# Kernel tuning notes

Measured on AMD Instinct MI355X. Metric: run time of the kernel, lower is better.

Reference implementation:

```python
import jax, jax.numpy as jnp
import numpy as np

EMB = 512
H = 8
D = EMB // H
N_TOK = 2048
IN_EMB = 1024
SCALE = EMB ** 0.5  # note: original divides AFTER softmax
EPS = 1e-5


def _layer_norm(x, g, b):
    m = x.mean(-1, keepdims=True)
    v = ((x - m) ** 2).mean(-1, keepdims=True)
    return (x - m) / jnp.sqrt(v + EPS) * g + b


def _mhla(x, idx, Wq, bq, Wk, bk, Wv, bv):
    # x: [b, n, EMB]; idx: [n, k] int neighbor indices into token axis
    b, n, _ = x.shape
    def heads(y):
        return y.reshape(b, n, H, D).transpose(0, 2, 1, 3)  # b h n d
    q = heads(x @ Wq + bq)
    k = heads(x @ Wk + bk)
    v = heads(x @ Wv + bv)
    Kl = k[:, :, idx, :]  # b h n k d  (gather of local keys)
    Vl = v[:, :, idx, :]  # b h n k d
    energy = jnp.einsum('bhnd,bhnkd->bhnk', q, Kl)
    att = jax.nn.softmax(energy, axis=-1) / SCALE  # faithful: scale after softmax
    patch_att = att.sum(axis=(1, 3)).T  # [n, b] (sum over heads, neighbors; stacked over n)
    out = jnp.einsum('bhnk,bhnkd->bhnd', att, Vl)
    out = out.transpose(0, 2, 1, 3).reshape(b, n, EMB)
    return out, patch_att


def setup_inputs() -> dict:
    key = jax.random.key(0)
    ks = jax.random.split(key, 16)
    def p(k, shape, s=0.02):
        return jax.random.normal(k, shape, dtype=jnp.float32) * s
    inp = {
        'x': jax.random.normal(ks[0], (1, N_TOK, IN_EMB), dtype=jnp.float32),
        'A': jax.random.randint(ks[1], (1, N_TOK, 64), 0, N_TOK),
        'W_fc': p(ks[2], (IN_EMB, EMB)), 'b_fc': jnp.zeros((EMB,), jnp.float32),
        'Wq1': p(ks[3], (EMB, EMB)), 'bq1': jnp.zeros((EMB,), jnp.float32),
        'Wk1': p(ks[4], (EMB, EMB)), 'bk1': jnp.zeros((EMB,), jnp.float32),
        'Wv1': p(ks[5], (EMB, EMB)), 'bv1': jnp.zeros((EMB,), jnp.float32),
        'g1': jnp.ones((EMB,), jnp.float32), 'be1': jnp.zeros((EMB,), jnp.float32),
        'Wq2': p(ks[6], (EMB, EMB)), 'bq2': jnp.zeros((EMB,), jnp.float32),
        'Wk2': p(ks[7], (EMB, EMB)), 'bk2': jnp.zeros((EMB,), jnp.float32),
        'Wv2': p(ks[8], (EMB, EMB)), 'bv2': jnp.zeros((EMB,), jnp.float32),
        'g2': jnp.ones((EMB,), jnp.float32), 'be2': jnp.zeros((EMB,), jnp.float32),
    }
    return inp


def reference(x, A, W_fc, b_fc, Wq1, bq1, Wk1, bk1, Wv1, bv1, g1, be1,
              Wq2, bq2, Wk2, bk2, Wv2, bv2, g2, be2):
    embs = jax.nn.relu(x @ W_fc + b_fc)  # FeedForwardBlock (dropout p=0)
    idx = A[0]  # batch==1 as required by torch.squeeze semantics in original
    b1, _ = _mhla(embs, idx[:, :16], Wq1, bq1, Wk1, bk1, Wv1, bv1)
    b1 = _layer_norm(b1 + embs, g1, be1)
    b2, Att2 = _mhla(b1, idx[:, :64], Wq2, bq2, Wk2, bk2, Wv2, bv2)
    b2 = _layer_norm(b2 + b1, g2, be2)
    return b2, Att2
```

## Files before the change

kernel.cpp:

```cpp
#include <hip/hip_runtime.h>

#define SCALE 22.627416997969522f
#define LNEPS 1e-5f
#define NTOK 2048

using short8 = __attribute__((ext_vector_type(8))) short;
using f32x4  = __attribute__((ext_vector_type(4))) float;
typedef unsigned short u16;
using u16x4 = __attribute__((ext_vector_type(4))) u16;

static __device__ __forceinline__ u16 f2bf(float f){
  unsigned u = __builtin_bit_cast(unsigned, f);
  u += 0x7FFFu + ((u >> 16) & 1u);
  return (u16)(u >> 16);
}
static __device__ __forceinline__ float bf2f(u16 u){
  unsigned v = ((unsigned)u) << 16;
  return __builtin_bit_cast(float, v);
}

__global__ __launch_bounds__(256) void cvt_k(const float* __restrict__ src,
                                             u16* __restrict__ dst, int n)
{
  int i = (blockIdx.x * 256 + threadIdx.x) * 4;
  if (i >= n) return;
  float4 v = *(const float4*)(src + i);
  u16x4 o;
  o[0] = f2bf(v.x); o[1] = f2bf(v.y); o[2] = f2bf(v.z); o[3] = f2bf(v.w);
  *(u16x4*)(dst + i) = o;
}

__global__ __launch_bounds__(256) void tr_k(
    const float* __restrict__ Wfc,
    const float* __restrict__ W1, const float* __restrict__ W2,
    const float* __restrict__ W3, const float* __restrict__ W4,
    const float* __restrict__ W5, const float* __restrict__ W6,
    u16* __restrict__ Tfc,
    u16* __restrict__ T1, u16* __restrict__ T2, u16* __restrict__ T3,
    u16* __restrict__ T4, u16* __restrict__ T5, u16* __restrict__ T6)
{
  int z = blockIdx.z;
  const float* W; u16* T; int K, N;
  if (z == 0) { W = Wfc; T = Tfc; K = 1024; N = 512; }
  else {
    K = 512; N = 512;
    switch (z) {
      case 1: W = W1; T = T1; break;
      case 2: W = W2; T = T2; break;
      case 3: W = W3; T = T3; break;
      case 4: W = W4; T = T4; break;
      case 5: W = W5; T = T5; break;
      default: W = W6; T = T6; break;
    }
    if ((int)blockIdx.y >= 16) return;
  }
  __shared__ float tile[32][33];
  int n0 = blockIdx.x * 32, k0 = blockIdx.y * 32;
  int tx = threadIdx.x & 31, ty = threadIdx.x >> 5;
#pragma unroll
  for (int i = 0; i < 32; i += 8)
    tile[ty + i][tx] = W[(size_t)(k0 + ty + i) * N + n0 + tx];
  __syncthreads();
#pragma unroll
  for (int i = 0; i < 32; i += 8)
    T[(size_t)(n0 + ty + i) * K + k0 + tx] = f2bf(tile[tx][ty + i]);
}

template<bool RELU, bool SPLIT3>
__global__ __launch_bounds__(256) void gemm_k(
    const u16* __restrict__ A, int K,
    const u16* __restrict__ T0, const u16* __restrict__ T1, const u16* __restrict__ T2,
    const float* __restrict__ B0, const float* __restrict__ B1, const float* __restrict__ B2,
    float* __restrict__ C0f, u16* __restrict__ C0b,
    u16* __restrict__ C1, u16* __restrict__ C2)
{
  __shared__ u16 As[64*64];
  __shared__ u16 Bs[64*64];

  int bm = blockIdx.x;
  int nglob = blockIdx.y * 64;
  int sel  = SPLIT3 ? (nglob >> 9) : 0;
  int ncol = nglob & 511;
  const u16*   T  = (sel==0) ? T0 : (sel==1) ? T1 : T2;
  const float* Bv = (sel==0) ? B0 : (sel==1) ? B1 : B2;

  int t = threadIdx.x;
  int wave = t >> 6, lane = t & 63;
  int wm = (wave >> 1) * 32, wn = (wave & 1) * 32;
  int lr = lane & 15, kg = lane >> 4;

  int o0 = t*16, o1 = 4096 + t*16;
  int r0 = o0 >> 7, cb0 = o0 & 127;
  int r1 = o1 >> 7, cb1 = o1 & 127;
  const char* Ag0 = (const char*)(A + (size_t)(bm*64 + r0) * K) + cb0;
  const char* Ag1 = (const char*)(A + (size_t)(bm*64 + r1) * K) + cb1;
  const char* Bg0 = (const char*)(T + (size_t)(ncol  + r0) * K) + cb0;
  const char* Bg1 = (const char*)(T + (size_t)(ncol  + r1) * K) + cb1;
  char* Ad0 = (char*)As + r0*128 + (cb0 ^ ((r0 & 7) << 4));
  char* Ad1 = (char*)As + r1*128 + (cb1 ^ ((r1 & 7) << 4));
  char* Bd0 = (char*)Bs + r0*128 + (cb0 ^ ((r0 & 7) << 4));
  char* Bd1 = (char*)Bs + r1*128 + (cb1 ^ ((r1 & 7) << 4));

  int sw = (lr & 7) << 4;
  const char* Afr0 = (const char*)As + (wm + lr) * 128;
  const char* Afr1 = (const char*)As + (wm + 16 + lr) * 128;
  const char* Bfr0 = (const char*)Bs + (wn + lr) * 128;
  const char* Bfr1 = (const char*)Bs + (wn + 16 + lr) * 128;

  f32x4 acc[2][2] = {};

  short8 pa0 = *(const short8*)Ag0;
  short8 pa1 = *(const short8*)Ag1;
  short8 pb0 = *(const short8*)Bg0;
  short8 pb1 = *(const short8*)Bg1;

  for (int k0 = 0; k0 < K; k0 += 64) {
    __syncthreads();
    *(short8*)Ad0 = pa0;  *(short8*)Ad1 = pa1;
    *(short8*)Bd0 = pb0;  *(short8*)Bd1 = pb1;
    __syncthreads();
    int kn = k0 + 64;
    if (kn < K) {
      pa0 = *(const short8*)(Ag0 + kn*2);
      pa1 = *(const short8*)(Ag1 + kn*2);
      pb0 = *(const short8*)(Bg0 + kn*2);
      pb1 = *(const short8*)(Bg1 + kn*2);
    }
#pragma unroll
    for (int ks = 0; ks < 2; ++ks) {
      int cb = (ks*64 + kg*16) ^ sw;
      short8 af0 = *(const short8*)(Afr0 + cb);
      short8 af1 = *(const short8*)(Afr1 + cb);
      short8 bf0 = *(const short8*)(Bfr0 + cb);
      short8 bf1 = *(const short8*)(Bfr1 + cb);
      acc[0][0] = __builtin_amdgcn_mfma_f32_16x16x32_bf16(af0, bf0, acc[0][0], 0, 0, 0);
      acc[0][1] = __builtin_amdgcn_mfma_f32_16x16x32_bf16(af0, bf1, acc[0][1], 0, 0, 0);
      acc[1][0] = __builtin_amdgcn_mfma_f32_16x16x32_bf16(af1, bf0, acc[1][0], 0, 0, 0);
      acc[1][1] = __builtin_amdgcn_mfma_f32_16x16x32_bf16(af1, bf1, acc[1][1], 0, 0, 0);
    }
  }

#pragma unroll
  for (int mi = 0; mi < 2; ++mi)
#pragma unroll
    for (int ni = 0; ni < 2; ++ni) {
      int col = ncol + wn + ni*16 + lr;
      float bia = Bv[col];
#pragma unroll
      for (int r = 0; r < 4; ++r) {
        int row = bm*64 + wm + mi*16 + kg*4 + r;
        float vv = acc[mi][ni][r] + bia;
        if (RELU) vv = fmaxf(vv, 0.f);
        if (SPLIT3) {
          if (sel == 0) {
            C0b[(size_t)row*512 + col] = f2bf(vv);
          } else {
            u16* C = (sel == 1) ? C1 : C2;
            C[((size_t)(col >> 6) * NTOK + row) * 64 + (col & 63)] = f2bf(vv);
          }
        } else {
          C0f[(size_t)row*512 + col] = vv;
          C0b[(size_t)row*512 + col] = f2bf(vv);
        }
      }
    }
}

template<int KLOC>
__global__ __launch_bounds__(512, 4) void attn_k(
    const u16* __restrict__ Qb, const u16* __restrict__ Kh, const u16* __restrict__ Vh,
    const int* __restrict__ Aidx,
    const float* __restrict__ resid,
    const float* __restrict__ gma, const float* __restrict__ bta,
    float* __restrict__ outp, u16* __restrict__ outb, float* __restrict__ attOut)
{
  constexpr int NP = KLOC / 16;
  constexpr int NV = KLOC / 8;

  __shared__ float o_s[512];
  __shared__ int   idx_s[KLOC];
  __shared__ float red_s[16];

  int n = blockIdx.x;
  int t = threadIdx.x;
  int w = t >> 6;
  int lane = t & 63;

  if (t < KLOC) idx_s[t] = Aidx[(size_t)n*64 + t];
  __syncthreads();

  const u16* Kbase = Kh + (size_t)w * NTOK * 64;
  const u16* Vbase = Vh + (size_t)w * NTOK * 64;
  int jj = lane & 15, dq = lane >> 4;
  int jg = lane >> 3, dc = lane & 7;

  short8 vpre[NV];
#pragma unroll
  for (int p = 0; p < NV; ++p)
    vpre[p] = *(const short8*)(Vbase + (size_t)idx_s[p*8 + jg] * 64 + dc*8);

  float qreg[16];
  {
    const u16* qp = Qb + (size_t)n*512 + w*64 + dq*16;
    short8 qa = *(const short8*)qp;
    short8 qb2 = *(const short8*)(qp + 8);
#pragma unroll
    for (int i = 0; i < 8; ++i) {
      qreg[i]     = bf2f((u16)qa[i]);
      qreg[8 + i] = bf2f((u16)qb2[i]);
    }
  }

  float att[NP];
#pragma unroll
  for (int p = 0; p < NP; ++p) {
    const u16* kp = Kbase + (size_t)idx_s[p*16 + jj] * 64 + dq*16;
    short8 k0 = *(const short8*)kp;
    short8 k1 = *(const short8*)(kp + 8);
    float e = 0.f;
#pragma unroll
    for (int i = 0; i < 8; ++i) {
      e = fmaf(qreg[i],     bf2f((u16)k0[i]), e);
      e = fmaf(qreg[8 + i], bf2f((u16)k1[i]), e);
    }
    e += __shfl_xor(e, 16);
    e += __shfl_xor(e, 32);
    att[p] = e;
  }

  float mx = att[0];
#pragma unroll
  for (int p = 1; p < NP; ++p) mx = fmaxf(mx, att[p]);
  mx = fmaxf(mx, __shfl_xor(mx, 1)); mx = fmaxf(mx, __shfl_xor(mx, 2));
  mx = fmaxf(mx, __shfl_xor(mx, 4)); mx = fmaxf(mx, __shfl_xor(mx, 8));
  float s = 0.f;
#pragma unroll
  for (int p = 0; p < NP; ++p) { att[p] = __expf(att[p] - mx); s += att[p]; }
  s += __shfl_xor(s, 1); s += __shfl_xor(s, 2);
  s += __shfl_xor(s, 4); s += __shfl_xor(s, 8);
  float inv = 1.f / (s * SCALE);
#pragma unroll
  for (int p = 0; p < NP; ++p) att[p] *= inv;

  float vacc[8] = {0.f,0.f,0.f,0.f,0.f,0.f,0.f,0.f};
#pragma unroll
  for (int p = 0; p < NV; ++p) {
    float a = __shfl(att[p >> 1], (p & 1) * 8 + jg);
#pragma unroll
    for (int i = 0; i < 8; ++i)
      vacc[i] = fmaf(a, bf2f((u16)vpre[p][i]), vacc[i]);
  }
#pragma unroll
  for (int i = 0; i < 8; ++i) {
    vacc[i] += __shfl_xor(vacc[i], 8);
    vacc[i] += __shfl_xor(vacc[i], 16);
    vacc[i] += __shfl_xor(vacc[i], 32);
  }
  if (jg == 0) {
#pragma unroll
    for (int i = 0; i < 8; ++i)
      o_s[w*64 + dc*8 + i] = vacc[i];
  }
  __syncthreads();

  float x = o_s[t] + __builtin_nontemporal_load(resid + (size_t)n*512 + t);
  float su = x, sq = x * x;
  su += __shfl_xor(su, 1);  sq += __shfl_xor(sq, 1);
  su += __shfl_xor(su, 2);  sq += __shfl_xor(sq, 2);
  su += __shfl_xor(su, 4);  sq += __shfl_xor(sq, 4);
  su += __shfl_xor(su, 8);  sq += __shfl_xor(sq, 8);
  su += __shfl_xor(su, 16); sq += __shfl_xor(sq, 16);
  su += __shfl_xor(su, 32); sq += __shfl_xor(sq, 32);
  if (lane == 0) { red_s[w] = su; red_s[8 + w] = sq; }
  __syncthreads();
  float tot = 0.f, tots = 0.f;
#pragma unroll
  for (int i = 0; i < 8; ++i) { tot += red_s[i]; tots += red_s[8 + i]; }
  float mean = tot  * (1.0f/512.0f);
  float var  = tots * (1.0f/512.0f) - mean*mean;
  float rstd = rsqrtf(var + LNEPS);
  float y = (x - mean) * rstd * gma[t] + bta[t];
  __builtin_nontemporal_store(y, outp + (size_t)n*512 + t);
  if (outb != nullptr) outb[(size_t)n*512 + t] = f2bf(y);
  if (attOut != nullptr && t == 0) attOut[n] = 8.0f / SCALE;
}

extern "C" void kernel_launch(void* const* d_in, const int* in_sizes, int n_in,
                              void* d_out, int out_size, void* d_ws, size_t ws_size,
                              hipStream_t stream)
{
  const float* x   = (const float*)d_in[0];
  const int*   A   = (const int*)  d_in[1];
  const float* Wfc = (const float*)d_in[2];
  const float* bfc = (const float*)d_in[3];
  const float* Wq1 = (const float*)d_in[4];
  const float* bq1 = (const float*)d_in[5];
  const float* Wk1 = (const float*)d_in[6];
  const float* bk1 = (const float*)d_in[7];
  const float* Wv1 = (const float*)d_in[8];
  const float* bv1 = (const float*)d_in[9];
  const float* g1  = (const float*)d_in[10];
  const float* be1 = (const float*)d_in[11];
  const float* Wq2 = (const float*)d_in[12];
  const float* bq2 = (const float*)d_in[13];
  const float* Wk2 = (const float*)d_in[14];
  const float* bk2 = (const float*)d_in[15];
  const float* Wv2 = (const float*)d_in[16];
  const float* bv2 = (const float*)d_in[17];
  const float* g2  = (const float*)d_in[18];
  const float* be2 = (const float*)d_in[19];

  char* ws = (char*)d_ws;
  const size_t SZ = (size_t)NTOK*512;
  float* embs = (float*)ws;                    ws += SZ*4;
  float* b1   = (float*)ws;                    ws += SZ*4;
  u16* embs_b = (u16*)ws;                      ws += SZ*2;
  u16* b1_b   = (u16*)ws;                      ws += SZ*2;
  u16* qb     = (u16*)ws;                      ws += SZ*2;
  u16* kb     = (u16*)ws;                      ws += SZ*2;
  u16* vb     = (u16*)ws;                      ws += SZ*2;
  u16* xb     = (u16*)ws;                      ws += (size_t)NTOK*1024*2;
  u16* t_fc   = (u16*)ws;                      ws += (size_t)512*1024*2;
  u16* t_q1   = (u16*)ws;                      ws += (size_t)512*512*2;
  u16* t_k1   = (u16*)ws;                      ws += (size_t)512*512*2;
  u16* t_v1   = (u16*)ws;                      ws += (size_t)512*512*2;
  u16* t_q2   = (u16*)ws;                      ws += (size_t)512*512*2;
  u16* t_k2   = (u16*)ws;                      ws += (size_t)512*512*2;
  u16* t_v2   = (u16*)ws;                      ws += (size_t)512*512*2;

  float* out  = (float*)d_out;
  float* att2 = out + SZ;

  dim3 blk(256);
  cvt_k<<<dim3(2048), blk, 0, stream>>>(x, xb, NTOK*1024);
  tr_k<<<dim3(16, 32, 7), blk, 0, stream>>>(Wfc, Wq1, Wk1, Wv1, Wq2, Wk2, Wv2,
      t_fc, t_q1, t_k1, t_v1, t_q2, t_k2, t_v2);

  gemm_k<true,false><<<dim3(32, 8), blk, 0, stream>>>(xb, 1024,
      t_fc, nullptr, nullptr, bfc, nullptr, nullptr, embs, embs_b, nullptr, nullptr);
  gemm_k<false,true><<<dim3(32, 24), blk, 0, stream>>>(embs_b, 512,
      t_q1, t_k1, t_v1, bq1, bk1, bv1, nullptr, qb, kb, vb);
  attn_k<16><<<dim3(2048), dim3(512), 0, stream>>>(qb, kb, vb, A, embs, g1, be1, b1, b1_b, nullptr);
  gemm_k<false,true><<<dim3(32, 24), blk, 0, stream>>>(b1_b, 512,
      t_q2, t_k2, t_v2, bq2, bk2, bv2, nullptr, qb, kb, vb);
  attn_k<64><<<dim3(2048), dim3(512), 0, stream>>>(qb, kb, vb, A, b1, g2, be2, out, nullptr, att2);
}
```

Baseline: 172.2 us.

## Fuse all stages into one persistent megakernel with software grid barriers

Replaces the seven separate kernel launches (convert, transpose, three GEMMs, two attention passes) with a single persistent kernel of 256 blocks that runs each stage in turn, separated by atomic-counter grid barriers. Each 512-thread block runs two independent 256-thread GEMM engines, and each block handles 8 tokens per attention stage. Separate q/k/v buffers are added for the second layer. The aim is to remove launch gaps and tail effects between the small stages. In exchange it adds spin-barrier overhead, a memset launch, and lower parallelism in the attention stages (256 blocks instead of 2048, with occupancy hint 2 instead of 4). It also relies on all 256 blocks being co-resident.

```diff
diff --git a/kernel.cpp b/kernel.cpp
--- a/kernel.cpp
+++ b/kernel.cpp
@@ -3,6 +3,7 @@
 #define SCALE 22.627416997969522f
 #define LNEPS 1e-5f
 #define NTOK 2048
+#define NBLK 256
 
 using short8 = __attribute__((ext_vector_type(8))) short;
 using f32x4  = __attribute__((ext_vector_type(4))) float;
@@ -19,77 +20,46 @@
   return __builtin_bit_cast(float, v);
 }
 
-__global__ __launch_bounds__(256) void cvt_k(const float* __restrict__ src,
-                                             u16* __restrict__ dst, int n)
+struct MegaArgs {
+  const float* x; const int* A;
+  const float* Wfc; const float* bfc;
+  const float* Wq1; const float* bq1; const float* Wk1; const float* bk1;
+  const float* Wv1; const float* bv1; const float* g1;  const float* be1;
+  const float* Wq2; const float* bq2; const float* Wk2; const float* bk2;
+  const float* Wv2; const float* bv2; const float* g2;  const float* be2;
+  unsigned* ctr;
+  float* embs; u16* embs_b; float* b1; u16* b1_b;
+  u16* xb;
+  u16* qb; u16* kb; u16* vb;
+  u16* qb2; u16* kb2; u16* vb2;
+  u16* t_fc; u16* t_q1; u16* t_k1; u16* t_v1; u16* t_q2; u16* t_k2; u16* t_v2;
+  float* out; float* att2;
+};
+
+static __device__ __forceinline__ void gridbar(unsigned* ctr, unsigned target) {
+  __syncthreads();
+  if (threadIdx.x == 0) {
+    __threadfence();
+    __hip_atomic_fetch_add(ctr, 1u, __ATOMIC_ACQ_REL, __HIP_MEMORY_SCOPE_AGENT);
+    while (__hip_atomic_load(ctr, __ATOMIC_ACQUIRE, __HIP_MEMORY_SCOPE_AGENT) < target)
+      __builtin_amdgcn_s_sleep(2);
+    __threadfence();
+  }
+  __syncthreads();
+}
+
+static __device__ void gemm_engine(
+    int t2, const u16* __restrict__ A, int K,
+    const u16* __restrict__ T, const float* __restrict__ Bv,
+    int bm, int ncol, int mode,
+    float* __restrict__ Cf, u16* __restrict__ Cb,
+    u16* As, u16* Bs)
 {
-  int i = (blockIdx.x * 256 + threadIdx.x) * 4;
-  if (i >= n) return;
-  float4 v = *(const float4*)(src + i);
-  u16x4 o;
-  o[0] = f2bf(v.x); o[1] = f2bf(v.y); o[2] = f2bf(v.z); o[3] = f2bf(v.w);
-  *(u16x4*)(dst + i) = o;
-}
-
-__global__ __launch_bounds__(256) void tr_k(
-    const float* __restrict__ Wfc,
-    const float* __restrict__ W1, const float* __restrict__ W2,
-    const float* __restrict__ W3, const float* __restrict__ W4,
-    const float* __restrict__ W5, const float* __restrict__ W6,
-    u16* __restrict__ Tfc,
-    u16* __restrict__ T1, u16* __restrict__ T2, u16* __restrict__ T3,
-    u16* __restrict__ T4, u16* __restrict__ T5, u16* __restrict__ T6)
-{
-  int z = blockIdx.z;
-  const float* W; u16* T; int K, N;
-  if (z == 0) { W = Wfc; T = Tfc; K = 1024; N = 512; }
-  else {
-    K = 512; N = 512;
-    switch (z) {
-      case 1: W = W1; T = T1; break;
-      case 2: W = W2; T = T2; break;
-      case 3: W = W3; T = T3; break;
-      case 4: W = W4; T = T4; break;
-      case 5: W = W5; T = T5; break;
-      default: W = W6; T = T6; break;
-    }
-    if ((int)blockIdx.y >= 16) return;
-  }
-  __shared__ float tile[32][33];
-  int n0 = blockIdx.x * 32, k0 = blockIdx.y * 32;
-  int tx = threadIdx.x & 31, ty = threadIdx.x >> 5;
-#pragma unroll
-  for (int i = 0; i < 32; i += 8)
-    tile[ty + i][tx] = W[(size_t)(k0 + ty + i) * N + n0 + tx];
-  __syncthreads();
-#pragma unroll
-  for (int i = 0; i < 32; i += 8)
-    T[(size_t)(n0 + ty + i) * K + k0 + tx] = f2bf(tile[tx][ty + i]);
-}
-
-template<bool RELU, bool SPLIT3>
-__global__ __launch_bounds__(256) void gemm_k(
-    const u16* __restrict__ A, int K,
-    const u16* __restrict__ T0, const u16* __restrict__ T1, const u16* __restrict__ T2,
-    const float* __restrict__ B0, const float* __restrict__ B1, const float* __restrict__ B2,
-    float* __restrict__ C0f, u16* __restrict__ C0b,
-    u16* __restrict__ C1, u16* __restrict__ C2)
-{
-  __shared__ u16 As[64*64];
-  __shared__ u16 Bs[64*64];
-
-  int bm = blockIdx.x;
-  int nglob = blockIdx.y * 64;
-  int sel  = SPLIT3 ? (nglob >> 9) : 0;
-  int ncol = nglob & 511;
-  const u16*   T  = (sel==0) ? T0 : (sel==1) ? T1 : T2;
-  const float* Bv = (sel==0) ? B0 : (sel==1) ? B1 : B2;
-
-  int t = threadIdx.x;
-  int wave = t >> 6, lane = t & 63;
+  int wave = t2 >> 6, lane = t2 & 63;
   int wm = (wave >> 1) * 32, wn = (wave & 1) * 32;
   int lr = lane & 15, kg = lane >> 4;
 
-  int o0 = t*16, o1 = 4096 + t*16;
+  int o0 = t2*16, o1 = 4096 + t2*16;
   int r0 = o0 >> 7, cb0 = o0 & 127;
   int r1 = o1 >> 7, cb1 = o1 & 127;
   const char* Ag0 = (const char*)(A + (size_t)(bm*64 + r0) * K) + cb0;
@@ -150,42 +120,36 @@
       for (int r = 0; r < 4; ++r) {
         int row = bm*64 + wm + mi*16 + kg*4 + r;
         float vv = acc[mi][ni][r] + bia;
-        if (RELU) vv = fmaxf(vv, 0.f);
-        if (SPLIT3) {
-          if (sel == 0) {
-            C0b[(size_t)row*512 + col] = f2bf(vv);
-          } else {
-            u16* C = (sel == 1) ? C1 : C2;
-            C[((size_t)(col >> 6) * NTOK + row) * 64 + (col & 63)] = f2bf(vv);
-          }
+        if (mode == 0) {
+          vv = fmaxf(vv, 0.f);
+          Cf[(size_t)row*512 + col] = vv;
+          Cb[(size_t)row*512 + col] = f2bf(vv);
+        } else if (mode == 1) {
+          Cb[(size_t)row*512 + col] = f2bf(vv);
         } else {
-          C0f[(size_t)row*512 + col] = vv;
-          C0b[(size_t)row*512 + col] = f2bf(vv);
+          Cb[((size_t)(col >> 6) * NTOK + row) * 64 + (col & 63)] = f2bf(vv);
         }
       }
     }
 }
 
 template<int KLOC>
-__global__ __launch_bounds__(512, 4) void attn_k(
-    const u16* __restrict__ Qb, const u16* __restrict__ Kh, const u16* __restrict__ Vh,
-    const int* __restrict__ Aidx,
+static __device__ void attn_token(
+    int n, const u16* __restrict__ Qb, const u16* __restrict__ Kh,
+    const u16* __restrict__ Vh, const int* __restrict__ Aidx,
     const float* __restrict__ resid,
     const float* __restrict__ gma, const float* __restrict__ bta,
-    float* __restrict__ outp, u16* __restrict__ outb, float* __restrict__ attOut)
+    float* __restrict__ outp, u16* __restrict__ outb, float* __restrict__ attOut,
+    float* o_s, int* idx_s, float* red_s)
 {
   constexpr int NP = KLOC / 16;
   constexpr int NV = KLOC / 8;
 
-  __shared__ float o_s[512];
-  __shared__ int   idx_s[KLOC];
-  __shared__ float red_s[16];
-
-  int n = blockIdx.x;
   int t = threadIdx.x;
   int w = t >> 6;
   int lane = t & 63;
 
+  __syncthreads();
   if (t < KLOC) idx_s[t] = Aidx[(size_t)n*64 + t];
   __syncthreads();
 
@@ -285,63 +249,148 @@
   if (attOut != nullptr && t == 0) attOut[n] = 8.0f / SCALE;
 }
 
+__global__ __launch_bounds__(512, 2) void mega_k(MegaArgs p)
+{
+  __shared__ u16   As[2][4096];
+  __shared__ u16   Bs[2][4096];
+  __shared__ float ttile[32*33];
+  __shared__ float o_s[512];
+  __shared__ int   idx_s[64];
+  __shared__ float red_s[16];
+
+  const int t = threadIdx.x;
+  const int b = blockIdx.x;
+  const int eng = t >> 8, t2 = t & 255;
+  const int eid = b * 2 + eng;
+
+  {
+    int tid = b * 512 + t;
+#pragma unroll
+    for (int r = 0; r < 4; ++r) {
+      int i = (tid + r * 131072) << 2;
+      float4 v = *(const float4*)(p.x + i);
+      u16x4 o;
+      o[0] = f2bf(v.x); o[1] = f2bf(v.y); o[2] = f2bf(v.z); o[3] = f2bf(v.w);
+      *(u16x4*)(p.xb + i) = o;
+    }
+  }
+  {
+    int tx = t & 31, ty = t >> 5;
+    for (int j = 0; j < 8; ++j) {
+      int tt = b + j * 256;
+      const float* W; u16* T; int K, N, bx, by;
+      if (tt < 512) { W = p.Wfc; T = p.t_fc; K = 1024; N = 512; bx = tt & 15; by = tt >> 4; }
+      else {
+        int t3 = tt - 512; int z = t3 >> 8; int rr = t3 & 255;
+        K = 512; N = 512; bx = rr & 15; by = rr >> 4;
+        switch (z) {
+          case 0: W = p.Wq1; T = p.t_q1; break;
+          case 1: W = p.Wk1; T = p.t_k1; break;
+          case 2: W = p.Wv1; T = p.t_v1; break;
+          case 3: W = p.Wq2; T = p.t_q2; break;
+          case 4: W = p.Wk2; T = p.t_k2; break;
+          default: W = p.Wv2; T = p.t_v2; break;
+        }
+      }
+      int n0 = bx * 32, k0 = by * 32;
+      __syncthreads();
+#pragma unroll
+      for (int i = 0; i < 32; i += 16)
+        ttile[(ty + i) * 33 + tx] = W[(size_t)(k0 + ty + i) * N + n0 + tx];
+      __syncthreads();
+#pragma unroll
+      for (int i = 0; i < 32; i += 16)
+        T[(size_t)(n0 + ty + i) * K + k0 + tx] = f2bf(ttile[tx * 33 + ty + i]);
+    }
+  }
+  gridbar(p.ctr, NBLK);
+
+  for (int tt = eid; tt < 256; tt += 512)
+    gemm_engine(t2, p.xb, 1024, p.t_fc, p.bfc, tt & 31, (tt >> 5) * 64, 0,
+                p.embs, p.embs_b, As[eng], Bs[eng]);
+  gridbar(p.ctr, 2 * NBLK);
+
+  for (int tt = eid; tt < 768; tt += 512) {
+    int sel = tt >> 8, w2 = tt & 255;
+    const u16*   T = sel == 0 ? p.t_q1 : sel == 1 ? p.t_k1 : p.t_v1;
+    const float* B = sel == 0 ? p.bq1  : sel == 1 ? p.bk1  : p.bv1;
+    u16*         C = sel == 0 ? p.qb   : sel == 1 ? p.kb   : p.vb;
+    gemm_engine(t2, p.embs_b, 512, T, B, w2 & 31, (w2 >> 5) * 64, sel == 0 ? 1 : 2,
+                nullptr, C, As[eng], Bs[eng]);
+  }
+  gridbar(p.ctr, 3 * NBLK);
+
+  for (int ii = 0; ii < 8; ++ii)
+    attn_token<16>(b + ii * 256, p.qb, p.kb, p.vb, p.A, p.embs, p.g1, p.be1,
+                   p.b1, p.b1_b, nullptr, o_s, idx_s, red_s);
+  gridbar(p.ctr, 4 * NBLK);
+
+  for (int tt = eid; tt < 768; tt += 512) {
+    int sel = tt >> 8, w2 = tt & 255;
+    const u16*   T = sel == 0 ? p.t_q2 : sel == 1 ? p.t_k2 : p.t_v2;
+    const float* B = sel == 0 ? p.bq2  : sel == 1 ? p.bk2  : p.bv2;
+    u16*         C = sel == 0 ? p.qb2  : sel == 1 ? p.kb2  : p.vb2;
+    gemm_engine(t2, p.b1_b, 512, T, B, w2 & 31, (w2 >> 5) * 64, sel == 0 ? 1 : 2,
+                nullptr, C, As[eng], Bs[eng]);
+  }
+  gridbar(p.ctr, 5 * NBLK);
+
+  for (int ii = 0; ii < 8; ++ii)
+    attn_token<64>(b + ii * 256, p.qb2, p.kb2, p.vb2, p.A, p.b1, p.g2, p.be2,
+                   p.out, nullptr, p.att2, o_s, idx_s, red_s);
+}
+
 extern "C" void kernel_launch(void* const* d_in, const int* in_sizes, int n_in,
                               void* d_out, int out_size, void* d_ws, size_t ws_size,
                               hipStream_t stream)
 {
-  const float* x   = (const float*)d_in[0];
-  const int*   A   = (const int*)  d_in[1];
-  const float* Wfc = (const float*)d_in[2];
-  const float* bfc = (const float*)d_in[3];
-  const float* Wq1 = (const float*)d_in[4];
-  const float* bq1 = (const float*)d_in[5];
-  const float* Wk1 = (const float*)d_in[6];
-  const float* bk1 = (const float*)d_in[7];
-  const float* Wv1 = (const float*)d_in[8];
-  const float* bv1 = (const float*)d_in[9];
-  const float* g1  = (const float*)d_in[10];
-  const float* be1 = (const float*)d_in[11];
-  const float* Wq2 = (const float*)d_in[12];
-  const float* bq2 = (const float*)d_in[13];
-  const float* Wk2 = (const float*)d_in[14];
-  const float* bk2 = (const float*)d_in[15];
-  const float* Wv2 = (const float*)d_in[16];
-  const float* bv2 = (const float*)d_in[17];
-  const float* g2  = (const float*)d_in[18];
-  const float* be2 = (const float*)d_in[19];
+  MegaArgs p;
+  p.x   = (const float*)d_in[0];
+  p.A   = (const int*)  d_in[1];
+  p.Wfc = (const float*)d_in[2];
+  p.bfc = (const float*)d_in[3];
+  p.Wq1 = (const float*)d_in[4];
+  p.bq1 = (const float*)d_in[5];
+  p.Wk1 = (const float*)d_in[6];
+  p.bk1 = (const float*)d_in[7];
+  p.Wv1 = (const float*)d_in[8];
+  p.bv1 = (const float*)d_in[9];
+  p.g1  = (const float*)d_in[10];
+  p.be1 = (const float*)d_in[11];
+  p.Wq2 = (const float*)d_in[12];
+  p.bq2 = (const float*)d_in[13];
+  p.Wk2 = (const float*)d_in[14];
+  p.bk2 = (const float*)d_in[15];
+  p.Wv2 = (const float*)d_in[16];
+  p.bv2 = (const float*)d_in[17];
+  p.g2  = (const float*)d_in[18];
+  p.be2 = (const float*)d_in[19];
 
   char* ws = (char*)d_ws;
-  const size_t SZ = (size_t)NTOK*512;
-  float* embs = (float*)ws;                    ws += SZ*4;
-  float* b1   = (float*)ws;                    ws += SZ*4;
-  u16* embs_b = (u16*)ws;                      ws += SZ*2;
-  u16* b1_b   = (u16*)ws;                      ws += SZ*2;
-  u16* qb     = (u16*)ws;                      ws += SZ*2;
-  u16* kb     = (u16*)ws;                      ws += SZ*2;
-  u16* vb     = (u16*)ws;                      ws += SZ*2;
-  u16* xb     = (u16*)ws;                      ws += (size_t)NTOK*1024*2;
-  u16* t_fc   = (u16*)ws;                      ws += (size_t)512*1024*2;
-  u16* t_q1   = (u16*)ws;                      ws += (size_t)512*512*2;
-  u16* t_k1   = (u16*)ws;                      ws += (size_t)512*512*2;
-  u16* t_v1   = (u16*)ws;                      ws += (size_t)512*512*2;
-  u16* t_q2   = (u16*)ws;                      ws += (size_t)512*512*2;
-  u16* t_k2   = (u16*)ws;                      ws += (size_t)512*512*2;
-  u16* t_v2   = (u16*)ws;                      ws += (size_t)512*512*2;
-
-  float* out  = (float*)d_out;
-  float* att2 = out + SZ;
-
-  dim3 blk(256);
-  cvt_k<<<dim3(2048), blk, 0, stream>>>(x, xb, NTOK*1024);
-  tr_k<<<dim3(16, 32, 7), blk, 0, stream>>>(Wfc, Wq1, Wk1, Wv1, Wq2, Wk2, Wv2,
-      t_fc, t_q1, t_k1, t_v1, t_q2, t_k2, t_v2);
-
-  gemm_k<true,false><<<dim3(32, 8), blk, 0, stream>>>(xb, 1024,
-      t_fc, nullptr, nullptr, bfc, nullptr, nullptr, embs, embs_b, nullptr, nullptr);
-  gemm_k<false,true><<<dim3(32, 24), blk, 0, stream>>>(embs_b, 512,
-      t_q1, t_k1, t_v1, bq1, bk1, bv1, nullptr, qb, kb, vb);
-  attn_k<16><<<dim3(2048), dim3(512), 0, stream>>>(qb, kb, vb, A, embs, g1, be1, b1, b1_b, nullptr);
-  gemm_k<false,true><<<dim3(32, 24), blk, 0, stream>>>(b1_b, 512,
-      t_q2, t_k2, t_v2, bq2, bk2, bv2, nullptr, qb, kb, vb);
-  attn_k<64><<<dim3(2048), dim3(512), 0, stream>>>(qb, kb, vb, A, b1, g2, be2, out, nullptr, att2);
-}
+  const size_t SZ = (size_t)NTOK * 512;
+  p.ctr    = (unsigned*)ws;  ws += 256;
+  p.embs   = (float*)ws;     ws += SZ * 4;
+  p.b1     = (float*)ws;     ws += SZ * 4;
+  p.embs_b = (u16*)ws;       ws += SZ * 2;
+  p.b1_b   = (u16*)ws;       ws += SZ * 2;
+  p.qb     = (u16*)ws;       ws += SZ * 2;
+  p.kb     = (u16*)ws;       ws += SZ * 2;
+  p.vb     = (u16*)ws;       ws += SZ * 2;
+  p.qb2    = (u16*)ws;       ws += SZ * 2;
+  p.kb2    = (u16*)ws;       ws += SZ * 2;
+  p.vb2    = (u16*)ws;       ws += SZ * 2;
+  p.xb     = (u16*)ws;       ws += (size_t)NTOK * 1024 * 2;
+  p.t_fc   = (u16*)ws;       ws += (size_t)512 * 1024 * 2;
+  p.t_q1   = (u16*)ws;       ws += (size_t)512 * 512 * 2;
+  p.t_k1   = (u16*)ws;       ws += (size_t)512 * 512 * 2;
+  p.t_v1   = (u16*)ws;       ws += (size_t)512 * 512 * 2;
+  p.t_q2   = (u16*)ws;       ws += (size_t)512 * 512 * 2;
+  p.t_k2   = (u16*)ws;       ws += (size_t)512 * 512 * 2;
+  p.t_v2   = (u16*)ws;       ws += (size_t)512 * 512 * 2;
+
+  p.out  = (float*)d_out;
+  p.att2 = p.out + SZ;
+
+  hipMemsetAsync(p.ctr, 0, 256, stream);
+  mega_k<<<dim3(NBLK), dim3(512), 0, stream>>>(p);
+}
```

Result: slower. 418.6 us (+143.1%).
